# Optimization experiments

Hardware: AMD Instinct MI355X
Metric: run time of the kernel (lower is better)

Reference implementation:

```python
import jax, jax.numpy as jnp
import numpy as np

B = 16384      # rays
H = 128        # field hidden dim


def setup_inputs() -> dict:
    key = jax.random.key(0)
    ks = jax.random.split(key, 8)
    origins = jax.random.normal(ks[0], (B, 3), dtype=jnp.float32)
    directions = jax.random.normal(ks[1], (B, 3), dtype=jnp.float32)
    directions = directions / jnp.linalg.norm(directions, axis=-1, keepdims=True)
    # Field: simple MLP 3 -> H -> H -> 4 (rgb + sigma)
    W1 = jax.random.normal(ks[2], (3, H), dtype=jnp.float32) * (1.0 / np.sqrt(3.0))
    b1 = jnp.zeros((H,), dtype=jnp.float32)
    W2 = jax.random.normal(ks[3], (H, H), dtype=jnp.float32) * (1.0 / np.sqrt(H))
    b2 = jnp.zeros((H,), dtype=jnp.float32)
    W3 = jax.random.normal(ks[4], (H, 4), dtype=jnp.float32) * (1.0 / np.sqrt(H))
    b3 = jnp.zeros((4,), dtype=jnp.float32)
    return {"origins": origins, "directions": directions,
            "W1": W1, "b1": b1, "W2": W2, "b2": b2, "W3": W3, "b3": b3,
            "near": 2, "far": 6, "num_samples": 64}


def _field(x, W1, b1, W2, b2, W3, b3):
    h = jax.nn.relu(x @ W1 + b1)
    h = jax.nn.relu(h @ W2 + b2)
    return h @ W3 + b3


def reference(origins, directions, W1, b1, W2, b2, W3, b3, near, far, num_samples):
    near = jnp.float32(near)
    far = jnp.float32(far)
    # 1. generate_samples: segment boundaries + midpoints along each ray
    depths = jnp.linspace(near, far, num_samples + 1)            # [S+1]
    midpoints = 0.5 * (depths[:-1] + depths[1:])                 # [S]
    # [B, S, 3] = origin + t * direction
    locs = origins[:, None, :] + midpoints[None, :, None] * directions[:, None, :]
    # 2. evaluate field
    f = _field(locs.reshape(-1, 3), W1, b1, W2, b2, W3, b3)
    f = f.reshape(origins.shape[0], num_samples, 4)
    # NOTE: source overwrites the sigmoid'd colors with raw outputs (faithful)
    colors = f[..., :3]                                          # [B, S, 3]
    sigma = f[..., 3]                                            # [B, S]
    # 3. alpha values
    delta = depths[1:] - depths[:-1]                             # [S]
    alphas = 1.0 - jnp.exp(-sigma * delta[None, :])              # [B, S]
    # 4. alpha compositing (black background)
    ones = jnp.ones_like(alphas[:, :1])
    transmittance = jnp.cumprod(jnp.concatenate([ones, 1.0 - alphas], axis=1), axis=1)[:, :-1]
    weights = alphas * transmittance                             # [B, S]
    radiance = jnp.sum(weights[..., None] * colors, axis=1)      # [B, 3]
    return radiance
```

## Files before the change

### kernel.cpp

```cpp
#include <hip/hip_runtime.h>


typedef _Float16 f16;
typedef __attribute__((ext_vector_type(2))) _Float16 h2v;
typedef __attribute__((ext_vector_type(8))) _Float16 half8;
typedef __attribute__((ext_vector_type(4))) float floatx4;

#define H 128
#define NS 64

static __device__ __forceinline__ h2v pkrtz(float a, float b) {
  return __builtin_bit_cast(h2v, __builtin_amdgcn_cvt_pkrtz(a, b));
}

template <int CTRL, int RM>
static __device__ __forceinline__ float dpp_add(float x) {
  int sh = __builtin_amdgcn_update_dpp(0, __builtin_bit_cast(int, x),
                                       CTRL, RM, 0xf, false);
  return x + __builtin_bit_cast(float, sh);
}

static __device__ __forceinline__ float wave_iscan(float x) {
  x = dpp_add<0x111, 0xf>(x);
  x = dpp_add<0x112, 0xf>(x);
  x = dpp_add<0x114, 0xf>(x);
  x = dpp_add<0x118, 0xf>(x);
  x = dpp_add<0x142, 0xa>(x);
  x = dpp_add<0x143, 0xc>(x);
  return x;
}

__global__ void nerf_setup(const float* __restrict__ W2, const float* __restrict__ W3,
                           f16* __restrict__ wsW2, f16* __restrict__ wsW3) {
  __shared__ __align__(16) f16 w2s[H * H];
  const int t = threadIdx.x;
  const int b = blockIdx.x;
  if (b < 8) {
    const float4* src = (const float4*)W2;
    #pragma unroll
    for (int i = 0; i < 16; ++i) {
      const float4 v = src[t + i * 256];
      const int e = (t + i * 256) * 4;
      h2v p0; p0[0] = (f16)v.x; p0[1] = (f16)v.y;
      h2v p1; p1[0] = (f16)v.z; p1[1] = (f16)v.w;
      *(h2v*)&w2s[e]     = p0;
      *(h2v*)&w2s[e + 2] = p1;
    }
    __syncthreads();
    #pragma unroll
    for (int j = 0; j < 4; ++j) {
      const int p = b * 1024 + j * 256 + t;
      const int j2 = p & 3, lane = (p >> 2) & 63, mt = (p >> 8) & 7, ks = p >> 11;
      const int l16 = lane & 15;
      const int k = ks * 32 + ((lane >> 4) * 8) + 2 * j2;
      const int n = 32 * (l16 >> 2) + mt * 4 + (l16 & 3);
      h2v pr; pr[0] = w2s[k * H + n]; pr[1] = w2s[(k + 1) * H + n];
      *(h2v*)&wsW2[2 * p] = pr;
    }
  } else {
    #pragma unroll
    for (int j = 0; j < 4; ++j) {
      const int u = j * 256 + t;
      const int j2 = u & 3, lane = (u >> 2) & 63, ks = u >> 8;
      const int c = lane & 15;
      const int k3 = 32 * (lane >> 4) + ks * 8 + 2 * j2;
      h2v pr;
      pr[0] = (c < 4) ? (f16)W3[k3 * 4 + c]       : (f16)0.0f;
      pr[1] = (c < 4) ? (f16)W3[(k3 + 1) * 4 + c] : (f16)0.0f;
      *(h2v*)&wsW3[2 * u] = pr;
    }
  }
}

__global__ __launch_bounds__(512, 4) void nerf_main(
    const float* __restrict__ origins, const float* __restrict__ dirs,
    const float* __restrict__ W1, const float* __restrict__ b1,
    const float* __restrict__ b2, const float* __restrict__ b3,
    const f16* __restrict__ ws,
    float* __restrict__ out)
{
  __shared__ __align__(16) half8 w_lds[2304];
  __shared__ __align__(16) float b2_lds[H];
  __shared__ __align__(16) f16   popd[8][2][H];
  __shared__ __align__(16) float f_lds[8][64][4];

  const int t = threadIdx.x;
  const int w = t >> 6, lane = t & 63, quad = lane >> 4, l16 = lane & 15;
  const float delta = 4.0f / NS;
  const int ray = blockIdx.x * 8 + w;

  {
    const uint4* src = (const uint4*)ws;
    uint4* dst = (uint4*)w_lds;
    #pragma unroll
    for (int i = 0; i < 4; ++i) dst[t + i * 512] = src[t + i * 512];
    if (t < 256) dst[t + 2048] = src[t + 2048];
    if (t < 32)  ((float4*)b2_lds)[t] = ((const float4*)b2)[t];
  }

  {
    const float o0 = origins[ray*3], o1 = origins[ray*3+1], o2 = origins[ray*3+2];
    const float d0 = dirs[ray*3],    d1 = dirs[ray*3+1],    d2 = dirs[ray*3+2];
    const int k0 = lane * 2;
    const float2 wr0 = *(const float2*)&W1[0*H + k0];
    const float2 wr1 = *(const float2*)&W1[1*H + k0];
    const float2 wr2 = *(const float2*)&W1[2*H + k0];
    const float2 bb  = *(const float2*)&b1[k0];
    float poa = fmaf(o2, wr2.x, fmaf(o1, wr1.x, fmaf(o0, wr0.x, bb.x)));
    float pob = fmaf(o2, wr2.y, fmaf(o1, wr1.y, fmaf(o0, wr0.y, bb.y)));
    float pda = fmaf(d2, wr2.x, fmaf(d1, wr1.x, d0 * wr0.x));
    float pdb = fmaf(d2, wr2.y, fmaf(d1, wr1.y, d0 * wr0.y));
    h2v po2; po2[0] = (f16)poa; po2[1] = (f16)pob;
    h2v pd2; pd2[0] = (f16)pda; pd2[1] = (f16)pdb;
    *(h2v*)&popd[w][0][k0] = po2;
    *(h2v*)&popd[w][1][k0] = pd2;
  }

  half8 hb[4][4];
  {
    const half8 z8 = (half8)(f16)0.0f;
    half8 m8[4];
    #pragma unroll
    for (int tr = 0; tr < 4; ++tr)
      m8[tr] = (half8)(f16)(2.0f + (tr*16 + l16 + 0.5f) * delta);
    #pragma unroll
    for (int ks = 0; ks < 4; ++ks) {
      const half8 po8 = *(const half8*)&popd[w][0][ks*32 + quad*8];
      const half8 pd8 = *(const half8*)&popd[w][1][ks*32 + quad*8];
      #pragma unroll
      for (int tr = 0; tr < 4; ++tr)
        hb[ks][tr] = __builtin_elementwise_max(pd8 * m8[tr] + po8, z8);
    }
  }

  __syncthreads();

  const half8* w2f = w_lds;
  const half8* w3f = w_lds + 2048;
  const h2v z2 = (h2v)(f16)0.0f;

  floatx4 acc3[4];
  {
    const float4 b3v = *(const float4*)&b3[0];
    #pragma unroll
    for (int tr = 0; tr < 4; ++tr) {
      acc3[tr][0] = b3v.x; acc3[tr][1] = b3v.y;
      acc3[tr][2] = b3v.z; acc3[tr][3] = b3v.w;
    }
  }

  #pragma unroll 1
  for (int it = 0; it < 4; ++it) {
    const int ks3 = (w + it) & 3;
    const int mt0 = 2 * ks3, mt1 = mt0 + 1;
    const float4 bA = *(const float4*)&b2_lds[quad*32 + ks3*8];
    const float4 bB = *(const float4*)&b2_lds[quad*32 + ks3*8 + 4];
    const half8 w3k = w3f[ks3*64 + lane];
    floatx4 accA[4], accB[4];
    #pragma unroll
    for (int tr = 0; tr < 4; ++tr) {
      accA[tr][0] = bA.x; accA[tr][1] = bA.y; accA[tr][2] = bA.z; accA[tr][3] = bA.w;
      accB[tr][0] = bB.x; accB[tr][1] = bB.y; accB[tr][2] = bB.z; accB[tr][3] = bB.w;
    }
    #pragma unroll
    for (int ks2 = 0; ks2 < 4; ++ks2) {
      const half8 wA = w2f[(ks2*8 + mt0)*64 + lane];
      const half8 wB = w2f[(ks2*8 + mt1)*64 + lane];
      #pragma unroll
      for (int tr = 0; tr < 4; ++tr) {
        accA[tr] = __builtin_amdgcn_mfma_f32_16x16x32_f16(wA, hb[ks2][tr], accA[tr], 0, 0, 0);
        accB[tr] = __builtin_amdgcn_mfma_f32_16x16x32_f16(wB, hb[ks2][tr], accB[tr], 0, 0, 0);
      }
    }
    #pragma unroll
    for (int tr = 0; tr < 4; ++tr) {
      h2v c0 = __builtin_elementwise_max(pkrtz(accA[tr][0], accA[tr][1]), z2);
      h2v c1 = __builtin_elementwise_max(pkrtz(accA[tr][2], accA[tr][3]), z2);
      h2v c2 = __builtin_elementwise_max(pkrtz(accB[tr][0], accB[tr][1]), z2);
      h2v c3 = __builtin_elementwise_max(pkrtz(accB[tr][2], accB[tr][3]), z2);
      half8 b = { c0[0], c0[1], c1[0], c1[1], c2[0], c2[1], c3[0], c3[1] };
      acc3[tr] = __builtin_amdgcn_mfma_f32_16x16x32_f16(w3k, b, acc3[tr], 0, 0, 0);
    }
  }

  if (quad == 0) {
    #pragma unroll
    for (int tr = 0; tr < 4; ++tr) {
      float4 fv;
      fv.x = acc3[tr][0]; fv.y = acc3[tr][1];
      fv.z = acc3[tr][2]; fv.w = acc3[tr][3];
      *(float4*)&f_lds[w][tr*16 + l16][0] = fv;
    }
  }

  {
    const float4 fv = *(const float4*)&f_lds[w][lane][0];
    const float sigma = fv.w;
    const float alpha = 1.0f - __expf(-sigma * delta);
    const float S  = wave_iscan(sigma);
    const float T  = __expf(-delta * (S - sigma));
    const float wt = alpha * T;
    const float sr = wave_iscan(wt * fv.x);
    const float sg = wave_iscan(wt * fv.y);
    const float sb = wave_iscan(wt * fv.z);
    if (lane == 63) {
      out[ray*3+0] = sr; out[ray*3+1] = sg; out[ray*3+2] = sb;
    }
  }
}

extern "C" void kernel_launch(void* const* d_in, const int* in_sizes, int n_in,
                              void* d_out, int out_size, void* d_ws, size_t ws_size,
                              hipStream_t stream) {
  const float* origins = (const float*)d_in[0];
  const float* dirs    = (const float*)d_in[1];
  const float* W1      = (const float*)d_in[2];
  const float* b1      = (const float*)d_in[3];
  const float* W2      = (const float*)d_in[4];
  const float* b2      = (const float*)d_in[5];
  const float* W3      = (const float*)d_in[6];
  const float* b3      = (const float*)d_in[7];
  float* out = (float*)d_out;

  f16* wsW2 = (f16*)d_ws;
  f16* wsW3 = wsW2 + 16384;

  nerf_setup<<<9, 256, 0, stream>>>(W2, W3, wsW2, wsW3);
  nerf_main<<<16384 / 8, 512, 0, stream>>>(
      origins, dirs, W1, b1, b2, b3, wsW2, out);
}
```

Before: 107.9 us.

## Fuse weight-prep setup kernel into main kernel with per-block LDS transpose

Removes the separate nerf_setup launch and its workspace round trip. Each block of the main kernel now loads fp32 W2 directly, converts it to fp16 into a swizzled LDS staging buffer, then gathers it into the MFMA fragment layout in LDS, and builds the W3 fragments itself. This saves one kernel launch and the dependency between two kernels. In exchange, all 2048 blocks redo the conversion and transpose, which adds global reads of fp32 weights, extra LDS traffic and an extra barrier, and raises LDS use, which may lower occupancy.

```diff
diff --git a/kernel.cpp b/kernel.cpp
--- a/kernel.cpp
+++ b/kernel.cpp
@@ -30,59 +30,19 @@
   return x;
 }
 
-__global__ void nerf_setup(const float* __restrict__ W2, const float* __restrict__ W3,
-                           f16* __restrict__ wsW2, f16* __restrict__ wsW3) {
-  __shared__ __align__(16) f16 w2s[H * H];
-  const int t = threadIdx.x;
-  const int b = blockIdx.x;
-  if (b < 8) {
-    const float4* src = (const float4*)W2;
-    #pragma unroll
-    for (int i = 0; i < 16; ++i) {
-      const float4 v = src[t + i * 256];
-      const int e = (t + i * 256) * 4;
-      h2v p0; p0[0] = (f16)v.x; p0[1] = (f16)v.y;
-      h2v p1; p1[0] = (f16)v.z; p1[1] = (f16)v.w;
-      *(h2v*)&w2s[e]     = p0;
-      *(h2v*)&w2s[e + 2] = p1;
-    }
-    __syncthreads();
-    #pragma unroll
-    for (int j = 0; j < 4; ++j) {
-      const int p = b * 1024 + j * 256 + t;
-      const int j2 = p & 3, lane = (p >> 2) & 63, mt = (p >> 8) & 7, ks = p >> 11;
-      const int l16 = lane & 15;
-      const int k = ks * 32 + ((lane >> 4) * 8) + 2 * j2;
-      const int n = 32 * (l16 >> 2) + mt * 4 + (l16 & 3);
-      h2v pr; pr[0] = w2s[k * H + n]; pr[1] = w2s[(k + 1) * H + n];
-      *(h2v*)&wsW2[2 * p] = pr;
-    }
-  } else {
-    #pragma unroll
-    for (int j = 0; j < 4; ++j) {
-      const int u = j * 256 + t;
-      const int j2 = u & 3, lane = (u >> 2) & 63, ks = u >> 8;
-      const int c = lane & 15;
-      const int k3 = 32 * (lane >> 4) + ks * 8 + 2 * j2;
-      h2v pr;
-      pr[0] = (c < 4) ? (f16)W3[k3 * 4 + c]       : (f16)0.0f;
-      pr[1] = (c < 4) ? (f16)W3[(k3 + 1) * 4 + c] : (f16)0.0f;
-      *(h2v*)&wsW3[2 * u] = pr;
-    }
-  }
-}
-
-__global__ __launch_bounds__(512, 4) void nerf_main(
+__global__ __launch_bounds__(512, 4) void nerf_all(
     const float* __restrict__ origins, const float* __restrict__ dirs,
     const float* __restrict__ W1, const float* __restrict__ b1,
-    const float* __restrict__ b2, const float* __restrict__ b3,
-    const f16* __restrict__ ws,
+    const float* __restrict__ W2, const float* __restrict__ b2,
+    const float* __restrict__ W3, const float* __restrict__ b3,
     float* __restrict__ out)
 {
-  __shared__ __align__(16) half8 w_lds[2304];
+  __shared__ __align__(16) half8 w_frag[2304];
   __shared__ __align__(16) float b2_lds[H];
   __shared__ __align__(16) f16   popd[8][2][H];
-  __shared__ __align__(16) float f_lds[8][64][4];
+  __shared__ __align__(16) char  uni[32768];
+
+  float (*f_lds)[64][4] = (float (*)[64][4])uni;
 
   const int t = threadIdx.x;
   const int w = t >> 6, lane = t & 63, quad = lane >> 4, l16 = lane & 15;
@@ -90,12 +50,34 @@
   const int ray = blockIdx.x * 8 + w;
 
   {
-    const uint4* src = (const uint4*)ws;
-    uint4* dst = (uint4*)w_lds;
-    #pragma unroll
-    for (int i = 0; i < 4; ++i) dst[t + i * 512] = src[t + i * 512];
-    if (t < 256) dst[t + 2048] = src[t + 2048];
-    if (t < 32)  ((float4*)b2_lds)[t] = ((const float4*)b2)[t];
+    const float4* src = (const float4*)W2;
+    #pragma unroll
+    for (int i = 0; i < 8; ++i) {
+      const int idx = t + i * 512;
+      const float4 v = src[idx];
+      const int k = idx >> 5, n0 = (idx & 31) * 4;
+      int byte0 = k * 256 + 2 * n0;
+      byte0 ^= ((n0 >> 5) & 3) << 5;
+      h2v p0; p0[0] = (f16)v.x; p0[1] = (f16)v.y;
+      h2v p1; p1[0] = (f16)v.z; p1[1] = (f16)v.w;
+      *(h2v*)(uni + byte0)     = p0;
+      *(h2v*)(uni + byte0 + 4) = p1;
+    }
+    if (t < 256) {
+      h2v* wf2 = (h2v*)w_frag;
+      #pragma unroll
+      for (int j = 0; j < 4; ++j) {
+        const int u = t + j * 256;
+        const int j2 = u & 3, lu = (u >> 2) & 63, ks = u >> 8;
+        const int c = lu & 15;
+        const int k3 = 32 * (lu >> 4) + ks * 8 + 2 * j2;
+        h2v pr;
+        pr[0] = (c < 4) ? (f16)W3[k3 * 4 + c]       : (f16)0.0f;
+        pr[1] = (c < 4) ? (f16)W3[(k3 + 1) * 4 + c] : (f16)0.0f;
+        wf2[8192 + u] = pr;
+      }
+    }
+    if (t < 32) ((float4*)b2_lds)[t] = ((const float4*)b2)[t];
   }
 
   {
@@ -116,6 +98,29 @@
     *(h2v*)&popd[w][1][k0] = pd2;
   }
 
+  __syncthreads();
+
+  {
+    #pragma unroll
+    for (int i = 0; i < 4; ++i) {
+      const int F = t + i * 512;
+      const int lf = F & 63, mt = (F >> 6) & 7, ks = F >> 9;
+      const int lf16 = lf & 15, g = lf >> 4;
+      const int K0 = ks * 32 + g * 8;
+      const int n = 32 * (lf16 >> 2) + mt * 4 + (lf16 & 3);
+      int rb = 2 * n;
+      rb ^= ((n >> 5) & 3) << 5;
+      rb += K0 * 256;
+      half8 fr;
+      #pragma unroll
+      for (int r = 0; r < 8; ++r)
+        fr[r] = *(const f16*)(uni + rb + r * 256);
+      w_frag[F] = fr;
+    }
+  }
+
+  __syncthreads();
+
   half8 hb[4][4];
   {
     const half8 z8 = (half8)(f16)0.0f;
@@ -133,10 +138,8 @@
     }
   }
 
-  __syncthreads();
-
-  const half8* w2f = w_lds;
-  const half8* w3f = w_lds + 2048;
+  const half8* w2f = w_frag;
+  const half8* w3f = w_frag + 2048;
   const h2v z2 = (h2v)(f16)0.0f;
 
   floatx4 acc3[4];
@@ -222,10 +225,7 @@
   const float* b3      = (const float*)d_in[7];
   float* out = (float*)d_out;
 
-  f16* wsW2 = (f16*)d_ws;
-  f16* wsW3 = wsW2 + 16384;
-
-  nerf_setup<<<9, 256, 0, stream>>>(W2, W3, wsW2, wsW3);
-  nerf_main<<<16384 / 8, 512, 0, stream>>>(
-      origins, dirs, W1, b1, b2, b3, wsW2, out);
-}
+  (void)d_ws; (void)ws_size;
+  nerf_all<<<16384 / 8, 512, 0, stream>>>(
+      origins, dirs, W1, b1, W2, b2, W3, b3, out);
+}
```

New measurement: 114.6 us. +6.2%, slower.
